# Kernel tuning notes

Hardware: AMD Instinct MI355X
Metric: run time of the kernel (lower is better)

The kernel has to match this reference:

```python
import jax, jax.numpy as jnp
import numpy as np

B, SQ, SK, D, H = 4, 2048, 2048, 1024, 16
HD = D // H


def setup_inputs() -> dict:
    key = jax.random.key(0)
    ks = jax.random.split(key, 12)
    s = 1.0 / np.sqrt(D)
    return {
        "query": jax.random.normal(ks[0], (B, SQ, D), jnp.float32),
        "key": jax.random.normal(ks[1], (B, SK, D), jnp.float32),
        "value": jax.random.normal(ks[2], (B, SK, D), jnp.float32),
        "key_padding_mask": jax.random.randint(ks[3], (B, SK), 0, 2, jnp.int32),
        "Wq": jax.random.uniform(ks[4], (D, D), jnp.float32, -s, s),
        "bq": jnp.zeros((D,), jnp.float32),
        "Wk": jax.random.uniform(ks[5], (D, D), jnp.float32, -s, s),
        "bk": jnp.zeros((D,), jnp.float32),
        "Wv": jax.random.uniform(ks[6], (D, D), jnp.float32, -s, s),
        "bv": jnp.zeros((D,), jnp.float32),
        "Wo": jax.random.uniform(ks[7], (D, D), jnp.float32, -s, s),
        "bo": jnp.zeros((D,), jnp.float32),
    }


def reference(query, key, value, key_padding_mask, Wq, bq, Wk, bk, Wv, bv, Wo, bo):
    scale = HD ** -0.5
    # projections: torch Linear is x @ W.T + b
    q = (query @ Wq.T + bq).reshape(B, SQ, H, HD).transpose(0, 2, 1, 3)  # [B,H,SQ,HD]
    k = (key @ Wk.T + bk).reshape(B, SK, H, HD).transpose(0, 2, 1, 3)    # [B,H,SK,HD]
    v = (value @ Wv.T + bv).reshape(B, SK, H, HD).transpose(0, 2, 1, 3)  # [B,H,SK,HD]
    scores = jnp.einsum("bhqd,bhkd->bhqk", q, k) * scale                  # [B,H,SQ,SK]
    mask = key_padding_mask[:, None, None, :] != 0                        # True = keep
    scores = jnp.where(mask, scores, -jnp.inf)
    attn = jax.nn.softmax(scores, axis=-1)
    # dropout is identity at inference (eval mode)
    out = jnp.einsum("bhqk,bhkd->bhqd", attn, v)                          # [B,H,SQ,HD]
    out = out.transpose(0, 2, 1, 3).reshape(B, SQ, D)
    return out @ Wo.T + bo
```

## Files before the change

kernel.cpp:

```cpp
#include <hip/hip_runtime.h>


typedef __bf16 bf16_t;
typedef __attribute__((ext_vector_type(2))) __bf16 bf16x2;
typedef __attribute__((ext_vector_type(4))) __bf16 bf16x4;
typedef __attribute__((ext_vector_type(8))) __bf16 bf16x8;
typedef __attribute__((ext_vector_type(4))) float f32x4;

#define MFMA16(a, b, c) __builtin_amdgcn_mfma_f32_16x16x32_bf16(a, b, c, 0, 0, 0)

__device__ __forceinline__ void gl_lds16(const void* g, void* l) {
  __builtin_amdgcn_global_load_lds(
      (const __attribute__((address_space(1))) unsigned int*)g,
      (__attribute__((address_space(3))) unsigned int*)l, 16, 0, 0);
}

__device__ __forceinline__ bf16x2 cvt_pk_bf16(float a, float b) {
#if __has_builtin(__builtin_amdgcn_cvt_pk_bf16_f32)
  return __builtin_amdgcn_cvt_pk_bf16_f32(a, b);
#else
  bf16x2 r;
  r[0] = (bf16_t)a;
  r[1] = (bf16_t)b;
  return r;
#endif
}

__global__ void wconv_kernel(const float* __restrict__ Wq, const float* __restrict__ Wk,
                             const float* __restrict__ Wv, const float* __restrict__ Wo,
                             bf16_t* __restrict__ out) {
  const int m = blockIdx.y;
  const float* src = (m == 0) ? Wq : (m == 1) ? Wk : (m == 2) ? Wv : Wo;
  bf16_t* dst = out + (size_t)m * (1024 * 1024);
  const int idx = (blockIdx.x * 256 + threadIdx.x) * 4;
  float4 v = *(const float4*)(src + idx);
  bf16x4 pk;
  pk[0] = (bf16_t)v.x; pk[1] = (bf16_t)v.y; pk[2] = (bf16_t)v.z; pk[3] = (bf16_t)v.w;
  *(bf16x4*)(dst + idx) = pk;
}

__global__ __launch_bounds__(256, 2) void proj_kernel(
    const float* __restrict__ Aq, const float* __restrict__ Ak, const float* __restrict__ Av,
    const bf16_t* __restrict__ W16,
    const float* __restrict__ bq, const float* __restrict__ bk, const float* __restrict__ bv,
    bf16_t* __restrict__ q16, bf16_t* __restrict__ k16, bf16_t* __restrict__ vt16) {
  __shared__ __align__(16) bf16_t As[2][8192];
  __shared__ __align__(16) bf16_t Bs[2][8192];

  const int z = blockIdx.z;
  const float* A = (z == 0) ? Aq : (z == 1) ? Ak : Av;
  const bf16_t* Bw = W16 + (size_t)z * 1048576;
  const float* bias = (z == 0) ? bq : (z == 1) ? bk : bv;

  const int tid = threadIdx.x;
  const int lane = tid & 63, wave = tid >> 6;
  const int fm = lane & 15, quad = lane >> 4;
  const int wr = wave >> 1, wc = wave & 1;
  const int m0 = blockIdx.x * 128, n0 = blockIdx.y * 128;

  f32x4 acc[4][4];
#pragma unroll
  for (int i = 0; i < 4; ++i)
#pragma unroll
    for (int j = 0; j < 4; ++j) acc[i][j] = f32x4{0.f, 0.f, 0.f, 0.f};

  float4 areg[4][2];
  auto loadA = [&](int ks) {
#pragma unroll
    for (int it = 0; it < 4; ++it) {
      const int fid = wave * 4 + it;
      const int row = (fid >> 1) * 16 + fm;
      const int col = (fid & 1) * 32 + quad * 8;
      const float* s = A + (size_t)(m0 + row) * 1024 + ks * 64 + col;
      areg[it][0] = *(const float4*)s;
      areg[it][1] = *(const float4*)(s + 4);
    }
  };
  auto writeA = [&](int buf) {
#pragma unroll
    for (int it = 0; it < 4; ++it) {
      const int fid = wave * 4 + it;
      bf16x8 pk;
      bf16x2* p2 = (bf16x2*)&pk;
      p2[0] = cvt_pk_bf16(areg[it][0].x, areg[it][0].y);
      p2[1] = cvt_pk_bf16(areg[it][0].z, areg[it][0].w);
      p2[2] = cvt_pk_bf16(areg[it][1].x, areg[it][1].y);
      p2[3] = cvt_pk_bf16(areg[it][1].z, areg[it][1].w);
      *(bf16x8*)(As[buf] + fid * 512 + lane * 8) = pk;
    }
  };
  auto dmaB = [&](int ks, int buf) {
#pragma unroll
    for (int it = 0; it < 4; ++it) {
      const int fid = wave * 4 + it;
      const int row = (fid >> 1) * 16 + fm;
      const int col = (fid & 1) * 32 + quad * 8;
      gl_lds16(Bw + (size_t)(n0 + row) * 1024 + ks * 64 + col, Bs[buf] + fid * 512);
    }
  };

  loadA(0);
  writeA(0);
  dmaB(0, 0);

  for (int ks = 0; ks < 16; ++ks) {
    __syncthreads();
    if (ks < 15) {
      loadA(ks + 1);
      dmaB(ks + 1, (ks + 1) & 1);
    }
    const bf16_t* Ab = As[ks & 1];
    const bf16_t* Bb = Bs[ks & 1];
#pragma unroll
    for (int u = 0; u < 2; ++u) {
      bf16x8 af[4], bfr[4];
#pragma unroll
      for (int i = 0; i < 4; ++i)
        af[i] = *(const bf16x8*)(Ab + ((4 * wr + i) * 2 + u) * 512 + lane * 8);
#pragma unroll
      for (int j = 0; j < 4; ++j)
        bfr[j] = *(const bf16x8*)(Bb + ((4 * wc + j) * 2 + u) * 512 + lane * 8);
#pragma unroll
      for (int i = 0; i < 4; ++i)
#pragma unroll
        for (int j = 0; j < 4; ++j) acc[i][j] = MFMA16(af[i], bfr[j], acc[i][j]);
    }
    if (ks < 15) writeA((ks + 1) & 1);
  }

  float bval[4];
#pragma unroll
  for (int j = 0; j < 4; ++j) bval[j] = bias[n0 + wc * 64 + j * 16 + fm];

  bf16_t* outp = (z == 0) ? q16 : (z == 1) ? k16 : vt16;
#pragma unroll
  for (int i = 0; i < 4; ++i) {
#pragma unroll
    for (int j = 0; j < 4; ++j) {
      const int col = n0 + wc * 64 + j * 16 + fm;
#pragma unroll
      for (int r = 0; r < 4; ++r) {
        const int row = m0 + wr * 64 + i * 16 + quad * 4 + r;
        const float v = acc[i][j][r] + bval[j];
        if (z != 2) {
          outp[(size_t)row * 1024 + col] = (bf16_t)v;
        } else {
          const int bb = row >> 11, sk = row & 2047;
          const int tt = sk >> 7, L128 = sk & 127;
          const int c = L128 >> 5, hf = (L128 >> 4) & 1;
          const int qd = (L128 >> 2) & 3, rr = L128 & 3;
          const int hh = col >> 6, hd = col & 63;
          const int nt = hd >> 4, fv = hd & 15;
          const size_t idx = (((size_t)(bb * 16 + hh)) << 17) + tt * 8192 +
                             (nt * 4 + c) * 512 + (qd * 16 + fv) * 8 + hf * 4 + rr;
          outp[idx] = (bf16_t)v;
        }
      }
    }
  }
}

__global__ __launch_bounds__(256, 2) void oproj_kernel(
    const bf16_t* __restrict__ A, const bf16_t* __restrict__ Bw,
    const float* __restrict__ bias, float* __restrict__ outp) {
  __shared__ __align__(16) bf16_t As[2][8192];
  __shared__ __align__(16) bf16_t Bs[2][8192];

  const int tid = threadIdx.x;
  const int lane = tid & 63, wave = tid >> 6;
  const int fm = lane & 15, quad = lane >> 4;
  const int wr = wave >> 1, wc = wave & 1;
  const int m0 = blockIdx.x * 128, n0 = blockIdx.y * 128;

  f32x4 acc[4][4];
#pragma unroll
  for (int i = 0; i < 4; ++i)
#pragma unroll
    for (int j = 0; j < 4; ++j) acc[i][j] = f32x4{0.f, 0.f, 0.f, 0.f};

  auto stage = [&](int ks, int buf) {
#pragma unroll
    for (int it = 0; it < 4; ++it) {
      const int fid = wave * 4 + it;
      const int row = (fid >> 1) * 16 + fm;
      const int col = (fid & 1) * 32 + quad * 8;
      gl_lds16(A + (size_t)(m0 + row) * 1024 + ks * 64 + col, As[buf] + fid * 512);
      gl_lds16(Bw + (size_t)(n0 + row) * 1024 + ks * 64 + col, Bs[buf] + fid * 512);
    }
  };

  stage(0, 0);
  for (int ks = 0; ks < 16; ++ks) {
    __syncthreads();
    if (ks < 15) stage(ks + 1, (ks + 1) & 1);
    const bf16_t* Ab = As[ks & 1];
    const bf16_t* Bb = Bs[ks & 1];
#pragma unroll
    for (int u = 0; u < 2; ++u) {
      bf16x8 af[4], bfr[4];
#pragma unroll
      for (int i = 0; i < 4; ++i)
        af[i] = *(const bf16x8*)(Ab + ((4 * wr + i) * 2 + u) * 512 + lane * 8);
#pragma unroll
      for (int j = 0; j < 4; ++j)
        bfr[j] = *(const bf16x8*)(Bb + ((4 * wc + j) * 2 + u) * 512 + lane * 8);
#pragma unroll
      for (int i = 0; i < 4; ++i)
#pragma unroll
        for (int j = 0; j < 4; ++j) acc[i][j] = MFMA16(af[i], bfr[j], acc[i][j]);
    }
  }

  float bval[4];
#pragma unroll
  for (int j = 0; j < 4; ++j) bval[j] = bias[n0 + wc * 64 + j * 16 + fm];
#pragma unroll
  for (int i = 0; i < 4; ++i)
#pragma unroll
    for (int j = 0; j < 4; ++j) {
      const int col = n0 + wc * 64 + j * 16 + fm;
#pragma unroll
      for (int r = 0; r < 4; ++r) {
        const int row = m0 + wr * 64 + i * 16 + quad * 4 + r;
        outp[(size_t)row * 1024 + col] = acc[i][j][r] + bval[j];
      }
    }
}

__global__ __launch_bounds__(256, 3) void attn_kernel(
    const bf16_t* __restrict__ q16, const bf16_t* __restrict__ k16,
    const bf16_t* __restrict__ vt16, const int* __restrict__ mask,
    bf16_t* __restrict__ o16) {
  __shared__ __align__(16) bf16_t Kb[2][8192];
  __shared__ __align__(16) bf16_t Vb[8192];
  __shared__ float mb[2][128];

  const int tid = threadIdx.x;
  const int lane = tid & 63, wave = tid >> 6;
  const int fm = lane & 15, quad = lane >> 4;
  const int qt = blockIdx.x, bh = blockIdx.y;
  const int b = bh >> 4, h = bh & 15;
  const float SC = 0.125f * 1.44269504f;

  bf16x8 aq[2][2];
#pragma unroll
  for (int i = 0; i < 2; ++i)
#pragma unroll
    for (int dc = 0; dc < 2; ++dc) {
      const int row = qt * 128 + (2 * wave + i) * 16 + fm;
      aq[i][dc] = *(const bf16x8*)(q16 + ((size_t)(b * 2048 + row)) * 1024 + h * 64 +
                                   dc * 32 + quad * 8);
    }

  auto dmaK = [&](int t, int buf) {
    const bf16_t* kb = k16 + ((size_t)(b * 2048 + t * 128)) * 1024 + h * 64;
#pragma unroll
    for (int s = 0; s < 4; ++s) {
      const int fid = wave * 4 + s;
      const int row = (fid >> 1) * 16 + fm;
      const int col = (fid & 1) * 32 + quad * 8;
      gl_lds16(kb + (size_t)row * 1024 + col, Kb[buf] + fid * 512);
    }
  };
  auto dmaV = [&](int t) {
    const bf16_t* vb = vt16 + ((size_t)bh << 17) + t * 8192;
#pragma unroll
    for (int s = 0; s < 4; ++s) {
      const int fid = wave * 4 + s;
      gl_lds16(vb + fid * 512 + lane * 8, Vb + fid * 512);
    }
  };
  auto stageM = [&](int t) {
    if (tid < 32) {
      int4 m4 = *(const int4*)(mask + b * 2048 + t * 128 + tid * 4);
      float4 f{m4.x ? 0.f : -1e30f, m4.y ? 0.f : -1e30f, m4.z ? 0.f : -1e30f,
               m4.w ? 0.f : -1e30f};
      *(float4*)&mb[t & 1][tid * 4] = f;
    }
  };

  f32x4 oacc[2][4];
#pragma unroll
  for (int i = 0; i < 2; ++i)
#pragma unroll
    for (int n = 0; n < 4; ++n) oacc[i][n] = f32x4{0.f, 0.f, 0.f, 0.f};
  f32x4 lacc[2] = {f32x4{0.f, 0.f, 0.f, 0.f}, f32x4{0.f, 0.f, 0.f, 0.f}};
  bf16x8 ones;
#pragma unroll
  for (int e = 0; e < 8; ++e) ones[e] = (bf16_t)1.0f;

  dmaK(0, 0);
  stageM(0);

  for (int t = 0; t < 16; ++t) {
    __syncthreads();
    dmaV(t);
    const bf16_t* K = Kb[t & 1];

    f32x4 sacc[2][8];
#pragma unroll
    for (int i = 0; i < 2; ++i)
#pragma unroll
      for (int j = 0; j < 8; ++j) sacc[i][j] = f32x4{0.f, 0.f, 0.f, 0.f};
#pragma unroll
    for (int j = 0; j < 8; ++j) {
#pragma unroll
      for (int dc = 0; dc < 2; ++dc) {
        bf16x8 kf = *(const bf16x8*)(K + (j * 2 + dc) * 512 + lane * 8);
        sacc[0][j] = MFMA16(kf, aq[0][dc], sacc[0][j]);
        sacc[1][j] = MFMA16(kf, aq[1][dc], sacc[1][j]);
      }
    }

    const float* mrow = mb[t & 1];
#pragma unroll
    for (int j = 0; j < 8; ++j) {
      f32x4 md = *(const f32x4*)&mrow[j * 16 + quad * 4];
#pragma unroll
      for (int i = 0; i < 2; ++i)
#pragma unroll
        for (int r = 0; r < 4; ++r)
          sacc[i][j][r] = __builtin_amdgcn_exp2f(fmaf(sacc[i][j][r], SC, md[r]));
    }
    __syncthreads();
    if (t < 15) {
      dmaK(t + 1, (t + 1) & 1);
      stageM(t + 1);
    }

#pragma unroll
    for (int c = 0; c < 4; ++c) {
      bf16x8 pf[2];
#pragma unroll
      for (int i = 0; i < 2; ++i) {
        bf16x2* p2 = (bf16x2*)&pf[i];
        p2[0] = cvt_pk_bf16(sacc[i][2 * c][0], sacc[i][2 * c][1]);
        p2[1] = cvt_pk_bf16(sacc[i][2 * c][2], sacc[i][2 * c][3]);
        p2[2] = cvt_pk_bf16(sacc[i][2 * c + 1][0], sacc[i][2 * c + 1][1]);
        p2[3] = cvt_pk_bf16(sacc[i][2 * c + 1][2], sacc[i][2 * c + 1][3]);
      }
#pragma unroll
      for (int n = 0; n < 4; ++n) {
        bf16x8 vv = *(const bf16x8*)(Vb + (n * 4 + c) * 512 + lane * 8);
        oacc[0][n] = MFMA16(pf[0], vv, oacc[0][n]);
        oacc[1][n] = MFMA16(pf[1], vv, oacc[1][n]);
      }
      lacc[0] = MFMA16(pf[0], ones, lacc[0]);
      lacc[1] = MFMA16(pf[1], ones, lacc[1]);
    }
  }

#pragma unroll
  for (int i = 0; i < 2; ++i) {
#pragma unroll
    for (int r = 0; r < 4; ++r) {
      const float inv = 1.0f / lacc[i][r];
      const int row = qt * 128 + wave * 32 + i * 16 + quad * 4 + r;
#pragma unroll
      for (int n = 0; n < 4; ++n) {
        o16[((size_t)(b * 2048 + row)) * 1024 + h * 64 + n * 16 + fm] =
            (bf16_t)(oacc[i][n][r] * inv);
      }
    }
  }
}

extern "C" void kernel_launch(void* const* d_in, const int* in_sizes, int n_in,
                              void* d_out, int out_size, void* d_ws, size_t ws_size,
                              hipStream_t stream) {
  const float* query = (const float*)d_in[0];
  const float* key   = (const float*)d_in[1];
  const float* value = (const float*)d_in[2];
  const int* mask    = (const int*)d_in[3];
  const float* Wq = (const float*)d_in[4];
  const float* bq = (const float*)d_in[5];
  const float* Wk = (const float*)d_in[6];
  const float* bk = (const float*)d_in[7];
  const float* Wv = (const float*)d_in[8];
  const float* bv = (const float*)d_in[9];
  const float* Wo = (const float*)d_in[10];
  const float* bo = (const float*)d_in[11];

  char* ws = (char*)d_ws;
  bf16_t* W16  = (bf16_t*)ws;
  bf16_t* q16  = (bf16_t*)(ws + (size_t)8 * 1024 * 1024);
  bf16_t* k16  = q16 + 8388608;
  bf16_t* vt16 = k16 + 8388608;
  bf16_t* o16  = vt16 + 8388608;

  wconv_kernel<<<dim3(1024, 4), 256, 0, stream>>>(Wq, Wk, Wv, Wo, W16);
  proj_kernel<<<dim3(64, 8, 3), 256, 0, stream>>>(query, key, value, W16, bq, bk, bv,
                                                  q16, k16, vt16);
  attn_kernel<<<dim3(16, 64), 256, 0, stream>>>(q16, k16, vt16, mask, o16);
  oproj_kernel<<<dim3(64, 8), 256, 0, stream>>>(o16, W16 + 3145728, bo, (float*)d_out);
}
```

Measured before the change: 465.2 us.

## Pre-convert activations to bf16, unify GEMMs into 256x128 tiles, double-buffer attention

Result: slower. 515.0 us (+10.7%).

```diff
diff --git a/kernel.cpp b/kernel.cpp
--- a/kernel.cpp
+++ b/kernel.cpp
@@ -26,37 +26,61 @@
 #endif
 }
 
-__global__ void wconv_kernel(const float* __restrict__ Wq, const float* __restrict__ Wk,
-                             const float* __restrict__ Wv, const float* __restrict__ Wo,
-                             bf16_t* __restrict__ out) {
-  const int m = blockIdx.y;
-  const float* src = (m == 0) ? Wq : (m == 1) ? Wk : (m == 2) ? Wv : Wo;
-  bf16_t* dst = out + (size_t)m * (1024 * 1024);
-  const int idx = (blockIdx.x * 256 + threadIdx.x) * 4;
-  float4 v = *(const float4*)(src + idx);
+__global__ void conv_kernel(const float* __restrict__ q, const float* __restrict__ k,
+                            const float* __restrict__ v, const float* __restrict__ Wq,
+                            const float* __restrict__ Wk, const float* __restrict__ Wv,
+                            const float* __restrict__ Wo, bf16_t* __restrict__ qf,
+                            bf16_t* __restrict__ kf, bf16_t* __restrict__ vf,
+                            bf16_t* __restrict__ W16) {
+  const int c = blockIdx.x;
+  const float* src;
+  bf16_t* dst;
+  if (c < 4096) {
+    const int w = c >> 10;
+    src = (w == 0) ? Wq : (w == 1) ? Wk : (w == 2) ? Wv : Wo;
+    dst = W16 + ((size_t)w << 20);
+    const size_t off = (size_t)(c & 1023) * 1024;
+    src += off;
+    dst += off;
+  } else {
+    const int a = c - 4096;
+    const int which = a >> 13;
+    src = (which == 0) ? q : (which == 1) ? k : v;
+    dst = (which == 0) ? qf : (which == 1) ? kf : vf;
+    const size_t off = (size_t)(a & 8191) * 1024;
+    src += off;
+    dst += off;
+  }
+  const int idx = threadIdx.x * 4;
+  float4 x = *(const float4*)(src + idx);
   bf16x4 pk;
-  pk[0] = (bf16_t)v.x; pk[1] = (bf16_t)v.y; pk[2] = (bf16_t)v.z; pk[3] = (bf16_t)v.w;
+  pk[0] = (bf16_t)x.x; pk[1] = (bf16_t)x.y; pk[2] = (bf16_t)x.z; pk[3] = (bf16_t)x.w;
   *(bf16x4*)(dst + idx) = pk;
 }
 
-__global__ __launch_bounds__(256, 2) void proj_kernel(
-    const float* __restrict__ Aq, const float* __restrict__ Ak, const float* __restrict__ Av,
-    const bf16_t* __restrict__ W16,
-    const float* __restrict__ bq, const float* __restrict__ bk, const float* __restrict__ bv,
-    bf16_t* __restrict__ q16, bf16_t* __restrict__ k16, bf16_t* __restrict__ vt16) {
-  __shared__ __align__(16) bf16_t As[2][8192];
-  __shared__ __align__(16) bf16_t Bs[2][8192];
+struct GArgs {
+  const void* A[3];
+  const bf16_t* Wz[3];
+  const float* bias[3];
+  void* out[3];
+  int mode[3];
+};
+
+template <bool A_F32>
+__global__ __launch_bounds__(512, 1) void gemm256(GArgs g) {
+  __shared__ __align__(16) bf16_t As[2][32 * 512];
+  __shared__ __align__(16) bf16_t Bs[2][16 * 512];
 
   const int z = blockIdx.z;
-  const float* A = (z == 0) ? Aq : (z == 1) ? Ak : Av;
-  const bf16_t* Bw = W16 + (size_t)z * 1048576;
-  const float* bias = (z == 0) ? bq : (z == 1) ? bk : bv;
+  const bf16_t* Bw = g.Wz[z];
+  const float* bias = g.bias[z];
+  const int mode = g.mode[z];
 
   const int tid = threadIdx.x;
   const int lane = tid & 63, wave = tid >> 6;
   const int fm = lane & 15, quad = lane >> 4;
   const int wr = wave >> 1, wc = wave & 1;
-  const int m0 = blockIdx.x * 128, n0 = blockIdx.y * 128;
+  const int M0 = blockIdx.x * 256, N0 = blockIdx.y * 128;
 
   f32x4 acc[4][4];
 #pragma unroll
@@ -66,12 +90,13 @@
 
   float4 areg[4][2];
   auto loadA = [&](int ks) {
+    const float* A = (const float*)g.A[z];
 #pragma unroll
     for (int it = 0; it < 4; ++it) {
-      const int fid = wave * 4 + it;
-      const int row = (fid >> 1) * 16 + fm;
-      const int col = (fid & 1) * 32 + quad * 8;
-      const float* s = A + (size_t)(m0 + row) * 1024 + ks * 64 + col;
+      const int afid = wave * 4 + it;
+      const int row = (afid >> 1) * 16 + fm;
+      const int col = (afid & 1) * 32 + quad * 8;
+      const float* s = A + (size_t)(M0 + row) * 1024 + ks * 64 + col;
       areg[it][0] = *(const float4*)s;
       areg[it][1] = *(const float4*)(s + 4);
     }
@@ -79,35 +104,55 @@
   auto writeA = [&](int buf) {
 #pragma unroll
     for (int it = 0; it < 4; ++it) {
-      const int fid = wave * 4 + it;
+      const int afid = wave * 4 + it;
       bf16x8 pk;
       bf16x2* p2 = (bf16x2*)&pk;
       p2[0] = cvt_pk_bf16(areg[it][0].x, areg[it][0].y);
       p2[1] = cvt_pk_bf16(areg[it][0].z, areg[it][0].w);
       p2[2] = cvt_pk_bf16(areg[it][1].x, areg[it][1].y);
       p2[3] = cvt_pk_bf16(areg[it][1].z, areg[it][1].w);
-      *(bf16x8*)(As[buf] + fid * 512 + lane * 8) = pk;
+      *(bf16x8*)(As[buf] + afid * 512 + lane * 8) = pk;
+    }
+  };
+  auto dmaA = [&](int ks, int buf) {
+    const bf16_t* A = (const bf16_t*)g.A[z];
+#pragma unroll
+    for (int it = 0; it < 4; ++it) {
+      const int afid = wave * 4 + it;
+      const int row = (afid >> 1) * 16 + fm;
+      const int col = (afid & 1) * 32 + quad * 8;
+      gl_lds16(A + (size_t)(M0 + row) * 1024 + ks * 64 + col, As[buf] + afid * 512);
     }
   };
   auto dmaB = [&](int ks, int buf) {
 #pragma unroll
-    for (int it = 0; it < 4; ++it) {
-      const int fid = wave * 4 + it;
-      const int row = (fid >> 1) * 16 + fm;
-      const int col = (fid & 1) * 32 + quad * 8;
-      gl_lds16(Bw + (size_t)(n0 + row) * 1024 + ks * 64 + col, Bs[buf] + fid * 512);
+    for (int it = 0; it < 2; ++it) {
+      const int bfid = wave * 2 + it;
+      const int row = (bfid >> 1) * 16 + fm;
+      const int col = (bfid & 1) * 32 + quad * 8;
+      gl_lds16(Bw + (size_t)(N0 + row) * 1024 + ks * 64 + col, Bs[buf] + bfid * 512);
     }
   };
 
-  loadA(0);
-  writeA(0);
-  dmaB(0, 0);
+  if constexpr (A_F32) {
+    loadA(0);
+    writeA(0);
+    dmaB(0, 0);
+  } else {
+    dmaA(0, 0);
+    dmaB(0, 0);
+  }
 
   for (int ks = 0; ks < 16; ++ks) {
     __syncthreads();
+    const int nb = (ks + 1) & 1;
     if (ks < 15) {
-      loadA(ks + 1);
-      dmaB(ks + 1, (ks + 1) & 1);
+      if constexpr (A_F32) {
+        loadA(ks + 1);
+      } else {
+        dmaA(ks + 1, nb);
+      }
+      dmaB(ks + 1, nb);
     }
     const bf16_t* Ab = As[ks & 1];
     const bf16_t* Bb = Bs[ks & 1];
@@ -125,25 +170,28 @@
 #pragma unroll
         for (int j = 0; j < 4; ++j) acc[i][j] = MFMA16(af[i], bfr[j], acc[i][j]);
     }
-    if (ks < 15) writeA((ks + 1) & 1);
+    if constexpr (A_F32) {
+      if (ks < 15) writeA(nb);
+    }
   }
 
   float bval[4];
 #pragma unroll
-  for (int j = 0; j < 4; ++j) bval[j] = bias[n0 + wc * 64 + j * 16 + fm];
-
-  bf16_t* outp = (z == 0) ? q16 : (z == 1) ? k16 : vt16;
+  for (int j = 0; j < 4; ++j) bval[j] = bias[N0 + wc * 64 + j * 16 + fm];
+
 #pragma unroll
   for (int i = 0; i < 4; ++i) {
 #pragma unroll
     for (int j = 0; j < 4; ++j) {
-      const int col = n0 + wc * 64 + j * 16 + fm;
+      const int col = N0 + wc * 64 + j * 16 + fm;
 #pragma unroll
       for (int r = 0; r < 4; ++r) {
-        const int row = m0 + wr * 64 + i * 16 + quad * 4 + r;
+        const int row = M0 + wr * 64 + i * 16 + quad * 4 + r;
         const float v = acc[i][j][r] + bval[j];
-        if (z != 2) {
-          outp[(size_t)row * 1024 + col] = (bf16_t)v;
+        if (mode == 2) {
+          ((float*)g.out[z])[(size_t)row * 1024 + col] = v;
+        } else if (mode == 0) {
+          ((bf16_t*)g.out[z])[(size_t)row * 1024 + col] = (bf16_t)v;
         } else {
           const int bb = row >> 11, sk = row & 2047;
           const int tt = sk >> 7, L128 = sk & 127;
@@ -153,106 +201,43 @@
           const int nt = hd >> 4, fv = hd & 15;
           const size_t idx = (((size_t)(bb * 16 + hh)) << 17) + tt * 8192 +
                              (nt * 4 + c) * 512 + (qd * 16 + fv) * 8 + hf * 4 + rr;
-          outp[idx] = (bf16_t)v;
+          ((bf16_t*)g.out[z])[idx] = (bf16_t)v;
         }
       }
     }
   }
 }
 
-__global__ __launch_bounds__(256, 2) void oproj_kernel(
-    const bf16_t* __restrict__ A, const bf16_t* __restrict__ Bw,
-    const float* __restrict__ bias, float* __restrict__ outp) {
-  __shared__ __align__(16) bf16_t As[2][8192];
-  __shared__ __align__(16) bf16_t Bs[2][8192];
-
-  const int tid = threadIdx.x;
-  const int lane = tid & 63, wave = tid >> 6;
-  const int fm = lane & 15, quad = lane >> 4;
-  const int wr = wave >> 1, wc = wave & 1;
-  const int m0 = blockIdx.x * 128, n0 = blockIdx.y * 128;
-
-  f32x4 acc[4][4];
-#pragma unroll
-  for (int i = 0; i < 4; ++i)
-#pragma unroll
-    for (int j = 0; j < 4; ++j) acc[i][j] = f32x4{0.f, 0.f, 0.f, 0.f};
-
-  auto stage = [&](int ks, int buf) {
-#pragma unroll
-    for (int it = 0; it < 4; ++it) {
-      const int fid = wave * 4 + it;
-      const int row = (fid >> 1) * 16 + fm;
-      const int col = (fid & 1) * 32 + quad * 8;
-      gl_lds16(A + (size_t)(m0 + row) * 1024 + ks * 64 + col, As[buf] + fid * 512);
-      gl_lds16(Bw + (size_t)(n0 + row) * 1024 + ks * 64 + col, Bs[buf] + fid * 512);
-    }
-  };
-
-  stage(0, 0);
-  for (int ks = 0; ks < 16; ++ks) {
-    __syncthreads();
-    if (ks < 15) stage(ks + 1, (ks + 1) & 1);
-    const bf16_t* Ab = As[ks & 1];
-    const bf16_t* Bb = Bs[ks & 1];
-#pragma unroll
-    for (int u = 0; u < 2; ++u) {
-      bf16x8 af[4], bfr[4];
-#pragma unroll
-      for (int i = 0; i < 4; ++i)
-        af[i] = *(const bf16x8*)(Ab + ((4 * wr + i) * 2 + u) * 512 + lane * 8);
-#pragma unroll
-      for (int j = 0; j < 4; ++j)
-        bfr[j] = *(const bf16x8*)(Bb + ((4 * wc + j) * 2 + u) * 512 + lane * 8);
-#pragma unroll
-      for (int i = 0; i < 4; ++i)
-#pragma unroll
-        for (int j = 0; j < 4; ++j) acc[i][j] = MFMA16(af[i], bfr[j], acc[i][j]);
-    }
-  }
-
-  float bval[4];
-#pragma unroll
-  for (int j = 0; j < 4; ++j) bval[j] = bias[n0 + wc * 64 + j * 16 + fm];
-#pragma unroll
-  for (int i = 0; i < 4; ++i)
-#pragma unroll
-    for (int j = 0; j < 4; ++j) {
-      const int col = n0 + wc * 64 + j * 16 + fm;
-#pragma unroll
-      for (int r = 0; r < 4; ++r) {
-        const int row = m0 + wr * 64 + i * 16 + quad * 4 + r;
-        outp[(size_t)row * 1024 + col] = acc[i][j][r] + bval[j];
-      }
-    }
-}
-
-__global__ __launch_bounds__(256, 3) void attn_kernel(
+__global__ __launch_bounds__(256, 2) void attn_kernel(
     const bf16_t* __restrict__ q16, const bf16_t* __restrict__ k16,
     const bf16_t* __restrict__ vt16, const int* __restrict__ mask,
     bf16_t* __restrict__ o16) {
   __shared__ __align__(16) bf16_t Kb[2][8192];
-  __shared__ __align__(16) bf16_t Vb[8192];
+  __shared__ __align__(16) bf16_t Vb[2][8192];
   __shared__ float mb[2][128];
 
   const int tid = threadIdx.x;
   const int lane = tid & 63, wave = tid >> 6;
   const int fm = lane & 15, quad = lane >> 4;
-  const int qt = blockIdx.x, bh = blockIdx.y;
+  const int linear = blockIdx.x;
+  const int bh = (linear & 7) * 8 + ((linear >> 3) & 7);
+  const int qt = linear >> 6;
   const int b = bh >> 4, h = bh & 15;
   const float SC = 0.125f * 1.44269504f;
 
-  bf16x8 aq[2][2];
-#pragma unroll
-  for (int i = 0; i < 2; ++i)
-#pragma unroll
-    for (int dc = 0; dc < 2; ++dc) {
-      const int row = qt * 128 + (2 * wave + i) * 16 + fm;
-      aq[i][dc] = *(const bf16x8*)(q16 + ((size_t)(b * 2048 + row)) * 1024 + h * 64 +
-                                   dc * 32 + quad * 8);
-    }
-
-  auto dmaK = [&](int t, int buf) {
+  bf16x8 aq[2][2][2];
+#pragma unroll
+  for (int gq = 0; gq < 2; ++gq)
+#pragma unroll
+    for (int i = 0; i < 2; ++i)
+#pragma unroll
+      for (int dc = 0; dc < 2; ++dc) {
+        const int row = qt * 256 + gq * 128 + (2 * wave + i) * 16 + fm;
+        aq[gq][i][dc] = *(const bf16x8*)(q16 + ((size_t)(b * 2048 + row)) * 1024 +
+                                         h * 64 + dc * 32 + quad * 8);
+      }
+
+  auto stageKV = [&](int t, int buf) {
     const bf16_t* kb = k16 + ((size_t)(b * 2048 + t * 128)) * 1024 + h * 64;
 #pragma unroll
     for (int s = 0; s < 4; ++s) {
@@ -261,108 +246,106 @@
       const int col = (fid & 1) * 32 + quad * 8;
       gl_lds16(kb + (size_t)row * 1024 + col, Kb[buf] + fid * 512);
     }
-  };
-  auto dmaV = [&](int t) {
     const bf16_t* vb = vt16 + ((size_t)bh << 17) + t * 8192;
 #pragma unroll
     for (int s = 0; s < 4; ++s) {
       const int fid = wave * 4 + s;
-      gl_lds16(vb + fid * 512 + lane * 8, Vb + fid * 512);
-    }
-  };
-  auto stageM = [&](int t) {
+      gl_lds16(vb + fid * 512 + lane * 8, Vb[buf] + fid * 512);
+    }
     if (tid < 32) {
       int4 m4 = *(const int4*)(mask + b * 2048 + t * 128 + tid * 4);
       float4 f{m4.x ? 0.f : -1e30f, m4.y ? 0.f : -1e30f, m4.z ? 0.f : -1e30f,
                m4.w ? 0.f : -1e30f};
-      *(float4*)&mb[t & 1][tid * 4] = f;
+      *(float4*)&mb[buf][tid * 4] = f;
     }
   };
 
-  f32x4 oacc[2][4];
-#pragma unroll
-  for (int i = 0; i < 2; ++i)
-#pragma unroll
-    for (int n = 0; n < 4; ++n) oacc[i][n] = f32x4{0.f, 0.f, 0.f, 0.f};
-  f32x4 lacc[2] = {f32x4{0.f, 0.f, 0.f, 0.f}, f32x4{0.f, 0.f, 0.f, 0.f}};
+  f32x4 oacc[2][2][4];
+#pragma unroll
+  for (int gq = 0; gq < 2; ++gq)
+#pragma unroll
+    for (int i = 0; i < 2; ++i)
+#pragma unroll
+      for (int n = 0; n < 4; ++n) oacc[gq][i][n] = f32x4{0.f, 0.f, 0.f, 0.f};
+  f32x4 lacc[2][2];
+#pragma unroll
+  for (int gq = 0; gq < 2; ++gq)
+#pragma unroll
+    for (int i = 0; i < 2; ++i) lacc[gq][i] = f32x4{0.f, 0.f, 0.f, 0.f};
   bf16x8 ones;
 #pragma unroll
   for (int e = 0; e < 8; ++e) ones[e] = (bf16_t)1.0f;
 
-  dmaK(0, 0);
-  stageM(0);
-
+  stageKV(0, 0);
   for (int t = 0; t < 16; ++t) {
     __syncthreads();
-    dmaV(t);
+    if (t < 15) stageKV(t + 1, (t + 1) & 1);
     const bf16_t* K = Kb[t & 1];
-
-    f32x4 sacc[2][8];
+    const bf16_t* V = Vb[t & 1];
+    const float* mrow = mb[t & 1];
+
+#pragma unroll
+    for (int gq = 0; gq < 2; ++gq) {
+      f32x4 sacc[2][8];
+#pragma unroll
+      for (int i = 0; i < 2; ++i)
+#pragma unroll
+        for (int j = 0; j < 8; ++j) sacc[i][j] = f32x4{0.f, 0.f, 0.f, 0.f};
+#pragma unroll
+      for (int j = 0; j < 8; ++j) {
+#pragma unroll
+        for (int dc = 0; dc < 2; ++dc) {
+          bf16x8 kf = *(const bf16x8*)(K + (j * 2 + dc) * 512 + lane * 8);
+          sacc[0][j] = MFMA16(kf, aq[gq][0][dc], sacc[0][j]);
+          sacc[1][j] = MFMA16(kf, aq[gq][1][dc], sacc[1][j]);
+        }
+      }
+#pragma unroll
+      for (int j = 0; j < 8; ++j) {
+        f32x4 md = *(const f32x4*)&mrow[j * 16 + quad * 4];
+#pragma unroll
+        for (int i = 0; i < 2; ++i)
+#pragma unroll
+          for (int r = 0; r < 4; ++r)
+            sacc[i][j][r] = __builtin_amdgcn_exp2f(fmaf(sacc[i][j][r], SC, md[r]));
+      }
+#pragma unroll
+      for (int c = 0; c < 4; ++c) {
+        bf16x8 pf[2];
+#pragma unroll
+        for (int i = 0; i < 2; ++i) {
+          bf16x2* p2 = (bf16x2*)&pf[i];
+          p2[0] = cvt_pk_bf16(sacc[i][2 * c][0], sacc[i][2 * c][1]);
+          p2[1] = cvt_pk_bf16(sacc[i][2 * c][2], sacc[i][2 * c][3]);
+          p2[2] = cvt_pk_bf16(sacc[i][2 * c + 1][0], sacc[i][2 * c + 1][1]);
+          p2[3] = cvt_pk_bf16(sacc[i][2 * c + 1][2], sacc[i][2 * c + 1][3]);
+        }
+#pragma unroll
+        for (int n = 0; n < 4; ++n) {
+          bf16x8 vv = *(const bf16x8*)(V + (n * 4 + c) * 512 + lane * 8);
+          oacc[gq][0][n] = MFMA16(pf[0], vv, oacc[gq][0][n]);
+          oacc[gq][1][n] = MFMA16(pf[1], vv, oacc[gq][1][n]);
+        }
+        lacc[gq][0] = MFMA16(pf[0], ones, lacc[gq][0]);
+        lacc[gq][1] = MFMA16(pf[1], ones, lacc[gq][1]);
+      }
+    }
+  }
+
+#pragma unroll
+  for (int gq = 0; gq < 2; ++gq)
 #pragma unroll
     for (int i = 0; i < 2; ++i)
 #pragma unroll
-      for (int j = 0; j < 8; ++j) sacc[i][j] = f32x4{0.f, 0.f, 0.f, 0.f};
-#pragma unroll
-    for (int j = 0; j < 8; ++j) {
-#pragma unroll
-      for (int dc = 0; dc < 2; ++dc) {
-        bf16x8 kf = *(const bf16x8*)(K + (j * 2 + dc) * 512 + lane * 8);
-        sacc[0][j] = MFMA16(kf, aq[0][dc], sacc[0][j]);
-        sacc[1][j] = MFMA16(kf, aq[1][dc], sacc[1][j]);
-      }
-    }
-
-    const float* mrow = mb[t & 1];
-#pragma unroll
-    for (int j = 0; j < 8; ++j) {
-      f32x4 md = *(const f32x4*)&mrow[j * 16 + quad * 4];
-#pragma unroll
-      for (int i = 0; i < 2; ++i)
-#pragma unroll
-        for (int r = 0; r < 4; ++r)
-          sacc[i][j][r] = __builtin_amdgcn_exp2f(fmaf(sacc[i][j][r], SC, md[r]));
-    }
-    __syncthreads();
-    if (t < 15) {
-      dmaK(t + 1, (t + 1) & 1);
-      stageM(t + 1);
-    }
-
-#pragma unroll
-    for (int c = 0; c < 4; ++c) {
-      bf16x8 pf[2];
-#pragma unroll
-      for (int i = 0; i < 2; ++i) {
-        bf16x2* p2 = (bf16x2*)&pf[i];
-        p2[0] = cvt_pk_bf16(sacc[i][2 * c][0], sacc[i][2 * c][1]);
-        p2[1] = cvt_pk_bf16(sacc[i][2 * c][2], sacc[i][2 * c][3]);
-        p2[2] = cvt_pk_bf16(sacc[i][2 * c + 1][0], sacc[i][2 * c + 1][1]);
-        p2[3] = cvt_pk_bf16(sacc[i][2 * c + 1][2], sacc[i][2 * c + 1][3]);
-      }
-#pragma unroll
-      for (int n = 0; n < 4; ++n) {
-        bf16x8 vv = *(const bf16x8*)(Vb + (n * 4 + c) * 512 + lane * 8);
-        oacc[0][n] = MFMA16(pf[0], vv, oacc[0][n]);
-        oacc[1][n] = MFMA16(pf[1], vv, oacc[1][n]);
-      }
-      lacc[0] = MFMA16(pf[0], ones, lacc[0]);
-      lacc[1] = MFMA16(pf[1], ones, lacc[1]);
-    }
-  }
-
-#pragma unroll
-  for (int i = 0; i < 2; ++i) {
-#pragma unroll
-    for (int r = 0; r < 4; ++r) {
-      const float inv = 1.0f / lacc[i][r];
-      const int row = qt * 128 + wave * 32 + i * 16 + quad * 4 + r;
-#pragma unroll
-      for (int n = 0; n < 4; ++n) {
-        o16[((size_t)(b * 2048 + row)) * 1024 + h * 64 + n * 16 + fm] =
-            (bf16_t)(oacc[i][n][r] * inv);
-      }
-    }
-  }
+      for (int r = 0; r < 4; ++r) {
+        const float inv = 1.0f / lacc[gq][i][r];
+        const int row = qt * 256 + gq * 128 + wave * 32 + i * 16 + quad * 4 + r;
+#pragma unroll
+        for (int n = 0; n < 4; ++n) {
+          o16[((size_t)(b * 2048 + row)) * 1024 + h * 64 + n * 16 + fm] =
+              (bf16_t)(oacc[gq][i][n][r] * inv);
+        }
+      }
 }
 
 extern "C" void kernel_launch(void* const* d_in, const int* in_sizes, int n_in,
@@ -381,16 +364,41 @@
   const float* Wo = (const float*)d_in[10];
   const float* bo = (const float*)d_in[11];
 
+  const size_t MB = 1024 * 1024;
   char* ws = (char*)d_ws;
   bf16_t* W16  = (bf16_t*)ws;
-  bf16_t* q16  = (bf16_t*)(ws + (size_t)8 * 1024 * 1024);
-  bf16_t* k16  = q16 + 8388608;
-  bf16_t* vt16 = k16 + 8388608;
-  bf16_t* o16  = vt16 + 8388608;
-
-  wconv_kernel<<<dim3(1024, 4), 256, 0, stream>>>(Wq, Wk, Wv, Wo, W16);
-  proj_kernel<<<dim3(64, 8, 3), 256, 0, stream>>>(query, key, value, W16, bq, bk, bv,
-                                                  q16, k16, vt16);
-  attn_kernel<<<dim3(16, 64), 256, 0, stream>>>(q16, k16, vt16, mask, o16);
-  oproj_kernel<<<dim3(64, 8), 256, 0, stream>>>(o16, W16 + 3145728, bo, (float*)d_out);
-}
+  bf16_t* q16  = (bf16_t*)(ws + 8 * MB);
+  bf16_t* k16  = (bf16_t*)(ws + 24 * MB);
+  bf16_t* vt16 = (bf16_t*)(ws + 40 * MB);
+  const bool big = ws_size >= 104 * MB;
+  bf16_t* qf = (bf16_t*)(ws + 56 * MB);
+  bf16_t* kf = (bf16_t*)(ws + 72 * MB);
+  bf16_t* vf = (bf16_t*)(ws + 88 * MB);
+  bf16_t* o16 = big ? qf : (bf16_t*)(ws + 56 * MB);
+
+  conv_kernel<<<big ? 28672 : 4096, 256, 0, stream>>>(query, key, value, Wq, Wk, Wv, Wo,
+                                                      qf, kf, vf, W16);
+
+  GArgs pa;
+  pa.Wz[0] = W16; pa.Wz[1] = W16 + 1048576; pa.Wz[2] = W16 + 2097152;
+  pa.bias[0] = bq; pa.bias[1] = bk; pa.bias[2] = bv;
+  pa.out[0] = q16; pa.out[1] = k16; pa.out[2] = vt16;
+  pa.mode[0] = 0; pa.mode[1] = 0; pa.mode[2] = 1;
+  if (big) {
+    pa.A[0] = qf; pa.A[1] = kf; pa.A[2] = vf;
+    gemm256<false><<<dim3(32, 8, 3), 512, 0, stream>>>(pa);
+  } else {
+    pa.A[0] = query; pa.A[1] = key; pa.A[2] = value;
+    gemm256<true><<<dim3(32, 8, 3), 512, 0, stream>>>(pa);
+  }
+
+  attn_kernel<<<512, 256, 0, stream>>>(q16, k16, vt16, mask, o16);
+
+  GArgs oa;
+  oa.A[0] = o16; oa.Wz[0] = W16 + 3145728; oa.bias[0] = bo;
+  oa.out[0] = d_out; oa.mode[0] = 2;
+  oa.A[1] = oa.A[2] = nullptr; oa.Wz[1] = oa.Wz[2] = nullptr;
+  oa.bias[1] = oa.bias[2] = nullptr; oa.out[1] = oa.out[2] = nullptr;
+  oa.mode[1] = oa.mode[2] = 2;
+  gemm256<false><<<dim3(32, 8, 1), 512, 0, stream>>>(oa);
+}
```
